# Kernel optimization log

Measured on AMD Instinct MI355X. Metric: run time of the kernel, lower is better.

The kernel has to match this reference:

```python
import jax, jax.numpy as jnp
import numpy as np

HEADS = 4

def gat_layer(x, W, a_src, a_dst, bias, edge_index, n):
    # PyG-style GATConv with self-loops, heads averaged (concat=False) so out dim == hidden_dim
    H, C = a_src.shape
    h = (x @ W).reshape(n, H, C)                      # [N,H,C]
    loops = jnp.arange(n)
    src = jnp.concatenate([edge_index[0], loops])
    dst = jnp.concatenate([edge_index[1], loops])
    e = jax.nn.leaky_relu((h * a_src).sum(-1)[src] + (h * a_dst).sum(-1)[dst], 0.2)  # [E,H]
    m = jax.ops.segment_max(e, dst, num_segments=n)   # segment softmax over incoming edges
    ex = jnp.exp(e - m[dst])
    s = jax.ops.segment_sum(ex, dst, num_segments=n)
    alpha = ex / (s[dst] + 1e-16)
    out = jax.ops.segment_sum(alpha[:, :, None] * h[src], dst, num_segments=n)  # [N,H,C]
    return out.mean(axis=1) + bias

def setup_inputs() -> dict:
    key = jax.random.key(0)
    ks = jax.random.split(key, 24)
    Nd, Ni, Ne = 20000, 4096, 4096
    D_in, D = 512, 256
    n_int, n_emo = 64, 32
    inp = {}
    inp['dialogue_embeddings'] = jax.random.normal(ks[0], (Nd, D_in), jnp.float32)
    inp['intention_indices'] = jax.random.randint(ks[1], (Ni,), 0, n_int)
    inp['emotion_indices'] = jax.random.randint(ks[2], (Ne,), 0, n_emo)
    inp['dialogue_edge_index'] = jax.random.randint(ks[3], (2, Nd * 32), 0, Nd)
    inp['intention_edge_index'] = jax.random.randint(ks[4], (2, Ni * 16), 0, Ni)
    inp['emotion_edge_index'] = jax.random.randint(ks[5], (2, Ne * 16), 0, Ne)
    s = lambda k, shape: jax.random.normal(k, shape, jnp.float32) * 0.02
    inp['intention_emb'] = s(ks[6], (n_int, D))
    inp['emotion_emb'] = s(ks[7], (n_emo, D))
    inp['Wd'] = s(ks[8], (D_in, HEADS * D)); inp['a_src_d'] = s(ks[9], (HEADS, D)); inp['a_dst_d'] = s(ks[10], (HEADS, D)); inp['bd'] = jnp.zeros((D,), jnp.float32)
    inp['Wi'] = s(ks[11], (D, HEADS * D)); inp['a_src_i'] = s(ks[12], (HEADS, D)); inp['a_dst_i'] = s(ks[13], (HEADS, D)); inp['bi'] = jnp.zeros((D,), jnp.float32)
    inp['We'] = s(ks[14], (D, HEADS * D)); inp['a_src_e'] = s(ks[15], (HEADS, D)); inp['a_dst_e'] = s(ks[16], (HEADS, D)); inp['be'] = jnp.zeros((D,), jnp.float32)
    inp['W_dfc'] = s(ks[17], (D, D)); inp['b_dfc'] = jnp.zeros((D,), jnp.float32)
    inp['W_ifc'] = s(ks[18], (D, D)); inp['b_ifc'] = jnp.zeros((D,), jnp.float32)
    inp['W_efc'] = s(ks[19], (D, D)); inp['b_efc'] = jnp.zeros((D,), jnp.float32)
    inp['W_fc'] = s(ks[20], (3 * D, n_emo)); inp['b_fc'] = jnp.zeros((n_emo,), jnp.float32)
    return inp

def reference(dialogue_embeddings, intention_indices, emotion_indices,
              dialogue_edge_index, intention_edge_index, emotion_edge_index,
              intention_emb, emotion_emb,
              Wd, a_src_d, a_dst_d, bd, Wi, a_src_i, a_dst_i, bi,
              We, a_src_e, a_dst_e, be,
              W_dfc, b_dfc, W_ifc, b_ifc, W_efc, b_efc, W_fc, b_fc):
    Nd = dialogue_embeddings.shape[0]
    Ni = intention_indices.shape[0]
    Ne = emotion_indices.shape[0]
    ie = intention_emb[intention_indices]   # [Ni, D]
    ee = emotion_emb[emotion_indices]       # [Ne, D]
    d = gat_layer(dialogue_embeddings, Wd, a_src_d, a_dst_d, bd, dialogue_edge_index, Nd)
    d = jax.nn.relu(d @ W_dfc + b_dfc)
    i = gat_layer(ie, Wi, a_src_i, a_dst_i, bi, intention_edge_index, Ni)
    i = jax.nn.relu(i @ W_ifc + b_ifc)
    e = gat_layer(ee, We, a_src_e, a_dst_e, be, emotion_edge_index, Ne)
    e = jax.nn.relu(e @ W_efc + b_efc)
    iw = jax.nn.softmax(d @ i.T, axis=-1)   # [Nd, Ni]
    att_i = iw @ i                           # [Nd, D]
    ew = jax.nn.softmax(d @ e.T, axis=-1)   # [Nd, Ne]
    att_e = ew @ e                           # [Nd, D]
    inputs = jnp.concatenate([d, att_i, att_e], axis=-1)  # [Nd, 3D]
    return inputs @ W_fc + b_fc
```

## Files before the change

kernel.cpp:

```cpp
#include <hip/hip_runtime.h>
#include <hip/hip_bf16.h>
#include <math.h>

#define DEV static __device__ __forceinline__

typedef __attribute__((ext_vector_type(8))) short short8;
typedef __attribute__((ext_vector_type(4))) short short4v;
typedef __attribute__((ext_vector_type(4))) float f32x4;
typedef __attribute__((ext_vector_type(2))) long long2v;

DEV float bf2f(__hip_bfloat16 x) { return __bfloat162float(x); }
DEV __hip_bfloat16 f2bf(float x) { return __float2bfloat16(x); }
DEV short bfbits(float x) { __hip_bfloat16 h = __float2bfloat16(x); short s; __builtin_memcpy(&s, &h, 2); return s; }
DEV float b2f_bits(short s) { __hip_bfloat16 h; __builtin_memcpy(&h, &s, 2); return __bfloat162float(h); }
DEV float lrelu(float x) { return x > 0.f ? x : 0.2f * x; }

DEV float load_in(const void* p, long long i, bool f32) {
  return f32 ? ((const float*)p)[i] : bf2f(((const __hip_bfloat16*)p)[i]);
}

DEV long pack8_fp8(const float* f) {
  int lo = 0, hi = 0;
  lo = __builtin_amdgcn_cvt_pk_fp8_f32(f[0], f[1], lo, false);
  lo = __builtin_amdgcn_cvt_pk_fp8_f32(f[2], f[3], lo, true);
  hi = __builtin_amdgcn_cvt_pk_fp8_f32(f[4], f[5], hi, false);
  hi = __builtin_amdgcn_cvt_pk_fp8_f32(f[6], f[7], hi, true);
  return ((long)(unsigned)hi << 32) | (unsigned)lo;
}

DEV f32x4 mfma_fp8(long a, long b, f32x4 c) {
  return __builtin_amdgcn_mfma_f32_16x16x32_fp8_fp8(a, b, c, 0, 0, 0);
}

__global__ void HGAN_45148696215914_kernel() {}

__global__ void fill_k(__hip_bfloat16* __restrict__ p, float v, int n)
{
  int i = blockIdx.x * blockDim.x + threadIdx.x;
  if (i < n) p[i] = __float2bfloat16(v);
}

struct DetectArgs { const unsigned int* p[23]; int nw[23]; int id[23]; };

__global__ void detect_k(DetectArgs a, int* __restrict__ flags)
{
  __shared__ int cnt_sh;
  if (threadIdx.x == 0) cnt_sh = 0;
  __syncthreads();
  const unsigned int* w = a.p[blockIdx.x];
  int nwords = a.nw[blockIdx.x];
  int bad = 0;
  for (int i = threadIdx.x; i < nwords; i += blockDim.x) {
    unsigned int x = w[i];
    float v0 = __uint_as_float((x & 0xffffu) << 16);
    float v1 = __uint_as_float(x & 0xffff0000u);
    if (!(fabsf(v0) <= 1e4f)) bad++;
    if (!(fabsf(v1) <= 1e4f)) bad++;
  }
  atomicAdd(&cnt_sh, bad);
  __syncthreads();
  if (threadIdx.x == 0) flags[a.id[blockIdx.x]] = (cnt_sh > nwords / 4) ? 1 : 0;
}

struct CvArgs {
  const void* in[7]; const int* flag[7]; __hip_bfloat16* out[7];
  int K[7], N[7], NL[7], toff[7]; int nseg;
};

__global__ __launch_bounds__(256) void convtrN_k(CvArgs a)
{
  __shared__ __hip_bfloat16 t[32][33];
  int b = blockIdx.x;
  int s = 0;
  while (s + 1 < a.nseg && b >= a.toff[s + 1]) ++s;
  int ti = b - a.toff[s];
  int kb = a.K[s] >> 5;
  int bk = ti % kb, bn = ti / kb;
  const void* in = a.in[s];
  const int* flag = a.flag[s];
  __hip_bfloat16* out = a.out[s];
  int K = a.K[s], N = a.N[s];
  const bool f = flag && *flag;
  int lx = threadIdx.x & 31, ly = threadIdx.x >> 5;
  int gn = bn * 32 + lx;
#pragma unroll
  for (int rr = 0; rr < 32; rr += 8)
    t[rr + ly][lx] = (gn < N)
        ? f2bf(load_in(in, (long long)(bk * 32 + rr + ly) * N + gn, f))
        : f2bf(0.f);
  __syncthreads();
#pragma unroll
  for (int rr = 0; rr < 32; rr += 8)
    out[(size_t)(bn * 32 + rr + ly) * K + bk * 32 + lx] = t[lx][rr + ly];
}

DEV void mgemm_body(
    const void* A, const int* aflag, int lda, const int* idxA,
    const __hip_bfloat16* BT, void* C, int ldc,
    const void* bias, const int* biasflag, int relu,
    int permC, int M, int K, int Nlim, const int* cflag,
    int m0, int n0, __hip_bfloat16* Ash, __hip_bfloat16* Bsh)
{
  const bool af = aflag && *aflag;
  const bool bsf = biasflag && *biasflag;
  const bool cf = cflag && *cflag;
  const int tid = threadIdx.x;
  const int wv = tid >> 6, lane = tid & 63, qd = lane >> 4, lm = lane & 15;
  const int wr = wv >> 1, wc = wv & 1;

  f32x4 acc[4][4];
#pragma unroll
  for (int i = 0; i < 4; ++i)
    for (int j = 0; j < 4; ++j)
      for (int v = 0; v < 4; ++v) acc[i][j][v] = 0.f;

  for (int k0 = 0; k0 < K; k0 += 64) {
    __syncthreads();
    for (int u = tid; u < 1024; u += 256) {
      int r = u >> 3, cu = u & 7;
      int gm = m0 + r;
      short8 vv;
      if (gm < M) {
        long long row = idxA ? idxA[gm] : gm;
        long long basei = row * (long long)lda + k0 + cu * 8;
        if (af) {
          const float4* fp = (const float4*)((const float*)A + basei);
          float4 f0 = fp[0], f1 = fp[1];
          vv[0] = bfbits(f0.x); vv[1] = bfbits(f0.y);
          vv[2] = bfbits(f0.z); vv[3] = bfbits(f0.w);
          vv[4] = bfbits(f1.x); vv[5] = bfbits(f1.y);
          vv[6] = bfbits(f1.z); vv[7] = bfbits(f1.w);
        } else {
          vv = *(const short8*)((const __hip_bfloat16*)A + basei);
        }
      } else {
#pragma unroll
        for (int j = 0; j < 8; ++j) vv[j] = 0;
      }
      *(short8*)(&Ash[r * 72 + cu * 8]) = vv;
    }
    for (int u = tid; u < 1024; u += 256) {
      int r = u >> 3, cu = u & 7;
      *(short8*)(&Bsh[r * 72 + cu * 8]) =
          *(const short8*)(BT + (size_t)(n0 + r) * K + k0 + cu * 8);
    }
    __syncthreads();
#pragma unroll
    for (int ks = 0; ks < 2; ++ks) {
      short8 a[4], b[4];
#pragma unroll
      for (int i = 0; i < 4; ++i)
        a[i] = *(const short8*)(&Ash[(wr * 64 + i * 16 + lm) * 72 + ks * 32 + qd * 8]);
#pragma unroll
      for (int j = 0; j < 4; ++j)
        b[j] = *(const short8*)(&Bsh[(wc * 64 + j * 16 + lm) * 72 + ks * 32 + qd * 8]);
#pragma unroll
      for (int i = 0; i < 4; ++i)
#pragma unroll
        for (int j = 0; j < 4; ++j)
          acc[i][j] = __builtin_amdgcn_mfma_f32_16x16x32_bf16(a[i], b[j], acc[i][j], 0, 0, 0);
    }
  }
#pragma unroll
  for (int j = 0; j < 4; ++j) {
    int gn = n0 + wc * 64 + j * 16 + lm;
    if (gn >= Nlim) continue;
    float bv = bias ? load_in(bias, gn, bsf) : 0.f;
    int gcol = permC ? ((gn & 255) * 4 + (gn >> 8)) : gn;
#pragma unroll
    for (int i = 0; i < 4; ++i) {
#pragma unroll
      for (int v = 0; v < 4; ++v) {
        int gm = m0 + wr * 64 + i * 16 + qd * 4 + v;
        if (gm >= M) continue;
        float x = acc[i][j][v] + bv;
        if (relu) x = fmaxf(x, 0.f);
        long long idx = (long long)gm * ldc + gcol;
        if (cf) ((float*)C)[idx] = x;
        else    ((__hip_bfloat16*)C)[idx] = f2bf(x);
      }
    }
  }
}

__global__ __launch_bounds__(256) void mgemm_k(
    const void* __restrict__ A, const int* __restrict__ aflag, int lda,
    const int* __restrict__ idxA,
    const __hip_bfloat16* __restrict__ BT,
    void* __restrict__ C, int ldc,
    const void* __restrict__ bias, const int* __restrict__ biasflag, int relu,
    int permC, int M, int N, int K, int Nlim,
    const int* __restrict__ cflag)
{
  __shared__ __align__(16) __hip_bfloat16 Ash[128 * 72];
  __shared__ __align__(16) __hip_bfloat16 Bsh[128 * 72];
  (void)N;
  mgemm_body(A, aflag, lda, idxA, BT, C, ldc, bias, biasflag, relu,
             permC, M, K, Nlim, cflag,
             blockIdx.y * 128, blockIdx.x * 128, Ash, Bsh);
}

struct SegArgs {
  const void* A[3]; const int* aflag[3]; int lda[3]; const int* idxA[3];
  const __hip_bfloat16* BT[3]; void* C[3]; int ldc[3];
  const void* bias[3]; const int* bflag[3];
  int M[3]; int K[3]; int yoff[3];
  int relu, permC, Nlim;
};

__global__ __launch_bounds__(256) void mgemm_seg_k(SegArgs a)
{
  __shared__ __align__(16) __hip_bfloat16 Ash[128 * 72];
  __shared__ __align__(16) __hip_bfloat16 Bsh[128 * 72];
  int y = blockIdx.y;
  int s = (y >= a.yoff[2]) ? 2 : ((y >= a.yoff[1]) ? 1 : 0);
  mgemm_body(a.A[s], a.aflag[s], a.lda[s], a.idxA[s], a.BT[s], a.C[s], a.ldc[s],
             a.bias[s], a.bflag[s], a.relu, a.permC, a.M[s], a.K[s], a.Nlim,
             nullptr, (y - a.yoff[s]) * 128, blockIdx.x * 128, Ash, Bsh);
}

__global__ __launch_bounds__(256) void score3_k(
    const __hip_bfloat16* __restrict__ hI,
    const void* as1, const void* ad1, const int* sf1, const int* df1,
    const void* as2, const void* ad2, const int* sf2, const int* df2,
    const void* as3, const void* ad3, const int* sf3, const int* df3,
    int s1, int s2,
    float* __restrict__ ss, float* __restrict__ ds,
    int* __restrict__ cnt, int N)
{
  __shared__ float red[4][8];
  int n = blockIdx.x, c = threadIdx.x;
  if (c == 0) cnt[n] = 0;
  const void* a_src; const void* a_dst; const int* sfp; const int* dfp;
  if (n < s1)      { a_src = as1; a_dst = ad1; sfp = sf1; dfp = df1; }
  else if (n < s2) { a_src = as2; a_dst = ad2; sfp = sf2; dfp = df2; }
  else             { a_src = as3; a_dst = ad3; sfp = sf3; dfp = df3; }
  const bool sf = sfp && *sfp;
  const bool df = dfp && *dfp;
  short4v hv = *(const short4v*)(hI + (size_t)n * 1024 + c * 4);
  float h0 = b2f_bits(hv[0]), h1 = b2f_bits(hv[1]);
  float h2 = b2f_bits(hv[2]), h3 = b2f_bits(hv[3]);
  float r0 = h0 * load_in(a_src, 0 * 256 + c, sf);
  float r1 = h1 * load_in(a_src, 1 * 256 + c, sf);
  float r2 = h2 * load_in(a_src, 2 * 256 + c, sf);
  float r3 = h3 * load_in(a_src, 3 * 256 + c, sf);
  float t0 = h0 * load_in(a_dst, 0 * 256 + c, df);
  float t1 = h1 * load_in(a_dst, 1 * 256 + c, df);
  float t2 = h2 * load_in(a_dst, 2 * 256 + c, df);
  float t3 = h3 * load_in(a_dst, 3 * 256 + c, df);
#pragma unroll
  for (int o = 32; o > 0; o >>= 1) {
    r0 += __shfl_down(r0, o); r1 += __shfl_down(r1, o);
    r2 += __shfl_down(r2, o); r3 += __shfl_down(r3, o);
    t0 += __shfl_down(t0, o); t1 += __shfl_down(t1, o);
    t2 += __shfl_down(t2, o); t3 += __shfl_down(t3, o);
  }
  int wv = c >> 6, lane = c & 63;
  if (lane == 0) {
    red[wv][0] = r0; red[wv][1] = r1; red[wv][2] = r2; red[wv][3] = r3;
    red[wv][4] = t0; red[wv][5] = t1; red[wv][6] = t2; red[wv][7] = t3;
  }
  __syncthreads();
  if (c < 8) {
    float s = red[0][c] + red[1][c] + red[2][c] + red[3][c];
    if (c < 4) ss[n * 4 + c] = s;
    else       ds[n * 4 + (c - 4)] = s;
  }
}

__global__ void count3_k(const int* __restrict__ d1, int E1,
                         const int* __restrict__ d2, int E2, int o2,
                         const int* __restrict__ d3, int E3, int o3,
                         int* __restrict__ cnt)
{
  int k = blockIdx.x * blockDim.x + threadIdx.x;
  if (k < E1) atomicAdd(&cnt[d1[k]], 1);
  else if (k < E1 + E2) atomicAdd(&cnt[d2[k - E1] + o2], 1);
  else if (k < E1 + E2 + E3) atomicAdd(&cnt[d3[k - E1 - E2] + o3], 1);
}

__global__ __launch_bounds__(1024) void scan1_k(
    const int* __restrict__ cnt, int* __restrict__ offp, int* __restrict__ bsum, int n)
{
  __shared__ int sh[1024];
  int idx = blockIdx.x * 1024 + (int)threadIdx.x;
  int v = (idx < n) ? cnt[idx] : 0;
  sh[threadIdx.x] = v;
  __syncthreads();
  for (int d = 1; d < 1024; d <<= 1) {
    int t = (threadIdx.x >= (unsigned)d) ? sh[threadIdx.x - d] : 0;
    __syncthreads();
    sh[threadIdx.x] += t;
    __syncthreads();
  }
  if (idx < n) offp[idx] = sh[threadIdx.x] - v;
  if (threadIdx.x == 1023) bsum[blockIdx.x] = sh[1023];
}

__global__ void scan3_k(int* __restrict__ offp, const int* __restrict__ bsum,
                        int* __restrict__ cur, int n, int nb)
{
  int i = blockIdx.x * blockDim.x + threadIdx.x;
  if (i < n) {
    int chunk = i >> 10;
    int pre = 0;
    for (int b = 0; b < chunk; ++b) pre += bsum[b];
    int v = offp[i] + pre;
    offp[i] = v;
    cur[i] = v;
    if (i == n - 1) {
      int tot = 0;
      for (int b = 0; b < nb; ++b) tot += bsum[b];
      offp[n] = tot;
    }
  }
}

__global__ void scatter3_k(const int* __restrict__ s1, const int* __restrict__ d1, int E1,
                           const int* __restrict__ s2, const int* __restrict__ d2, int E2, int o2,
                           const int* __restrict__ s3, const int* __restrict__ d3, int E3, int o3,
                           int* __restrict__ cur, int* __restrict__ srcs)
{
  int k = blockIdx.x * blockDim.x + threadIdx.x;
  if (k < E1) {
    int p = atomicAdd(&cur[d1[k]], 1);
    srcs[p] = s1[k];
  } else if (k < E1 + E2) {
    int kk = k - E1;
    int p = atomicAdd(&cur[d2[kk] + o2], 1);
    srcs[p] = s2[kk] + o2;
  } else if (k < E1 + E2 + E3) {
    int kk = k - E1 - E2;
    int p = atomicAdd(&cur[d3[kk] + o3], 1);
    srcs[p] = s3[kk] + o3;
  }
}

__global__ __launch_bounds__(256) void agg3_k(
    const __hip_bfloat16* __restrict__ hI,
    const float* __restrict__ ss, const float* __restrict__ ds,
    const int* __restrict__ offp, const int* __restrict__ srcs,
    const void* b1, const int* bf1,
    const void* b2, const int* bf2,
    const void* b3, const int* bf3,
    int s1, int s2,
    __hip_bfloat16* __restrict__ outp, int N)
{
  __shared__ int src_sh[64];
  __shared__ __align__(16) float w_sh[64][4];
  __shared__ float scale_sh[4];
  __shared__ float l_sh[4];
  __shared__ __align__(16) float pair_sh[128][8];
  int n = blockIdx.x;
  int c = threadIdx.x;
  int hd_w = c >> 6;
  int e_w  = c & 63;
  int half = c >> 7;
  int tc   = c & 127;
  int s0 = offp[n], deg = offp[n + 1] - s0;
  int total = deg + 1;
  float dsn = ds[n * 4 + hd_w];
  float m_run = -1e30f, l_run = 0.f;
  float A0[4] = {0.f, 0.f, 0.f, 0.f};
  float A1[4] = {0.f, 0.f, 0.f, 0.f};
  for (int base = 0; base < total; base += 64) {
    int cnt = min(64, total - base);
    __syncthreads();
    if (c < cnt) src_sh[c] = (base + c == 0) ? n : srcs[s0 + base + c - 1];
    __syncthreads();
    float val = -1e30f;
    if (e_w < cnt) val = lrelu(ss[src_sh[e_w] * 4 + hd_w] + dsn);
    float vmax = val;
#pragma unroll
    for (int o = 32; o > 0; o >>= 1) vmax = fmaxf(vmax, __shfl_xor(vmax, o));
    float newm = fmaxf(m_run, vmax);
    float p = (e_w < cnt) ? __expf(val - newm) : 0.f;
    float psum = p;
#pragma unroll
    for (int o = 32; o > 0; o >>= 1) psum += __shfl_xor(psum, o);
    float sc = __expf(m_run - newm);
    l_run = l_run * sc + psum;
    m_run = newm;
    w_sh[e_w][hd_w] = p;
    if (e_w == 0) scale_sh[hd_w] = sc;
    __syncthreads();
    float sc0 = scale_sh[0], sc1 = scale_sh[1], sc2 = scale_sh[2], sc3 = scale_sh[3];
    A0[0] *= sc0; A0[1] *= sc1; A0[2] *= sc2; A0[3] *= sc3;
    A1[0] *= sc0; A1[1] *= sc1; A1[2] *= sc2; A1[3] *= sc3;
    for (int e = half; e < cnt; e += 2) {
      short8 hv = *(const short8*)(hI + (size_t)src_sh[e] * 1024 + tc * 8);
      float4 w = *(const float4*)(&w_sh[e][0]);
      A0[0] += w.x * b2f_bits(hv[0]); A0[1] += w.y * b2f_bits(hv[1]);
      A0[2] += w.z * b2f_bits(hv[2]); A0[3] += w.w * b2f_bits(hv[3]);
      A1[0] += w.x * b2f_bits(hv[4]); A1[1] += w.y * b2f_bits(hv[5]);
      A1[2] += w.z * b2f_bits(hv[6]); A1[3] += w.w * b2f_bits(hv[7]);
    }
  }
  __syncthreads();
  if (e_w == 0) l_sh[hd_w] = l_run;
  if (half == 1) {
    *(float4*)(&pair_sh[tc][0]) = make_float4(A0[0], A0[1], A0[2], A0[3]);
    *(float4*)(&pair_sh[tc][4]) = make_float4(A1[0], A1[1], A1[2], A1[3]);
  }
  __syncthreads();
  if (half == 0) {
    float4 p0 = *(const float4*)(&pair_sh[tc][0]);
    float4 p1 = *(const float4*)(&pair_sh[tc][4]);
    A0[0] += p0.x; A0[1] += p0.y; A0[2] += p0.z; A0[3] += p0.w;
    A1[0] += p1.x; A1[1] += p1.y; A1[2] += p1.z; A1[3] += p1.w;
    const void* bias; const int* bfp;
    if (n < s1)      { bias = b1; bfp = bf1; }
    else if (n < s2) { bias = b2; bfp = bf2; }
    else             { bias = b3; bfp = bf3; }
    const bool bf = bfp && *bfp;
    float il0 = 1.f / (l_sh[0] + 1e-16f), il1 = 1.f / (l_sh[1] + 1e-16f);
    float il2 = 1.f / (l_sh[2] + 1e-16f), il3 = 1.f / (l_sh[3] + 1e-16f);
    float r0 = 0.25f * (A0[0] * il0 + A0[1] * il1 + A0[2] * il2 + A0[3] * il3);
    float r1 = 0.25f * (A1[0] * il0 + A1[1] * il1 + A1[2] * il2 + A1[3] * il3);
    outp[(size_t)n * 256 + 2 * tc]     = f2bf(r0 + load_in(bias, 2 * tc, bf));
    outp[(size_t)n * 256 + 2 * tc + 1] = f2bf(r1 + load_in(bias, 2 * tc + 1, bf));
  }
}

__global__ __launch_bounds__(256) void conv8_k(
    const __hip_bfloat16* __restrict__ in0, char* __restrict__ K8_0, char* __restrict__ KT8_0,
    const __hip_bfloat16* __restrict__ in1, char* __restrict__ K8_1, char* __restrict__ KT8_1,
    int Nk)
{
  __shared__ __align__(16) __hip_bfloat16 t[32][264];
  const __hip_bfloat16* in = blockIdx.y ? in1 : in0;
  char* K8  = blockIdx.y ? K8_1  : K8_0;
  char* KT8 = blockIdx.y ? KT8_1 : KT8_0;
  int kv0 = blockIdx.x * 32;
  int tid = threadIdx.x;
  for (int u = tid; u < 1024; u += 256) {
    int r = u >> 5, c = u & 31;
    *(short8*)(&t[r][c * 8]) = *(const short8*)(in + (size_t)(kv0 + r) * 256 + c * 8);
  }
  __syncthreads();
  for (int u = tid; u < 1024; u += 256) {
    int r = u >> 5, g = u & 31, pos = g * 8;
    int qd = pos >> 6, s = (pos >> 3) & 7;
    int d = s * 32 + qd * 8;
    float f[8];
#pragma unroll
    for (int j = 0; j < 8; ++j) f[j] = 16.f * bf2f(t[r][d + j]);
    *(long*)(K8 + (size_t)(kv0 + r) * 256 + pos) = pack8_fp8(f);
  }
  {
    int d = tid;
#pragma unroll
    for (int g = 0; g < 4; ++g) {
      float f[8];
#pragma unroll
      for (int j = 0; j < 8; ++j) f[j] = 16.f * bf2f(t[g * 8 + j][d]);
      *(long*)(KT8 + (size_t)d * Nk + kv0 + g * 8) = pack8_fp8(f);
    }
  }
}

__global__ __launch_bounds__(256, 2) void flashf8_k(
    const __hip_bfloat16* __restrict__ Q, int ldq,
    const char* __restrict__ K8_0, const char* __restrict__ KT8_0,
    const char* __restrict__ K8_1, const char* __restrict__ KT8_1,
    __hip_bfloat16* __restrict__ Out, int ldo,
    int M, int Nk)
{
  __shared__ __align__(16) char Ksh8[2][32 * 272];
  __shared__ __align__(16) char KTsh8[2][256 * 48];
  __shared__ __align__(16) char Psh8[4][32 * 40];
  const int att = blockIdx.y;
  const char* K8  = att ? K8_1  : K8_0;
  const char* KT8 = att ? KT8_1 : KT8_0;
  __hip_bfloat16* Outp = Out + att * 256;

  const int tid = threadIdx.x;
  const int wv = tid >> 6, lane = tid & 63;
  const int qd = lane >> 4, lm = lane & 15;
  const int r0 = blockIdx.x * 128 + wv * 32;
  char* Pw = Psh8[wv];

  const int kr0 = tid >> 4, kc = tid & 15;
  const int tr0 = tid >> 1, tcq = tid & 1;

  long qf8[2][8];
#pragma unroll
  for (int mf = 0; mf < 2; ++mf) {
    const bool ok = (r0 + mf * 16 + lm) < M;
    const __hip_bfloat16* qrow = Q + (size_t)(r0 + mf * 16 + lm) * ldq;
#pragma unroll
    for (int s = 0; s < 8; ++s) {
      float f[8];
      if (ok) {
        short8 qv = *(const short8*)(qrow + s * 32 + qd * 8);
#pragma unroll
        for (int j = 0; j < 8; ++j) f[j] = 16.f * b2f_bits(qv[j]);
      } else {
#pragma unroll
        for (int j = 0; j < 8; ++j) f[j] = 0.f;
      }
      qf8[mf][s] = pack8_fp8(f);
    }
  }

  f32x4 Oacc[2][16];
#pragma unroll
  for (int mf = 0; mf < 2; ++mf)
    for (int i = 0; i < 16; ++i)
      for (int v = 0; v < 4; ++v) Oacc[mf][i][v] = 0.f;
  float mrow[2] = {-1e30f, -1e30f}, lrow[2] = {0.f, 0.f};

  {
    short8 k0 = *(const short8*)(K8 + (size_t)kr0 * 256 + kc * 16);
    short8 k1 = *(const short8*)(K8 + (size_t)(kr0 + 16) * 256 + kc * 16);
    short8 t0 = *(const short8*)(KT8 + (size_t)tr0 * Nk + tcq * 16);
    short8 t1 = *(const short8*)(KT8 + (size_t)(tr0 + 128) * Nk + tcq * 16);
    *(short8*)(&Ksh8[0][kr0 * 272 + kc * 16]) = k0;
    *(short8*)(&Ksh8[0][(kr0 + 16) * 272 + kc * 16]) = k1;
    *(short8*)(&KTsh8[0][tr0 * 48 + tcq * 16]) = t0;
    *(short8*)(&KTsh8[0][(tr0 + 128) * 48 + tcq * 16]) = t1;
  }
  __syncthreads();

  int iter = 0;
  for (int n0 = 0; n0 < Nk; n0 += 32, ++iter) {
    const int cur = iter & 1, nxt = cur ^ 1;
    const bool havenext = (n0 + 32) < Nk;
    short8 pk0, pk1, pt0, pt1;
    if (havenext) {
      int nn = n0 + 32;
      pk0 = *(const short8*)(K8 + (size_t)(nn + kr0) * 256 + kc * 16);
      pk1 = *(const short8*)(K8 + (size_t)(nn + kr0 + 16) * 256 + kc * 16);
      pt0 = *(const short8*)(KT8 + (size_t)tr0 * Nk + nn + tcq * 16);
      pt1 = *(const short8*)(KT8 + (size_t)(tr0 + 128) * Nk + nn + tcq * 16);
    }
    const char* Kc  = Ksh8[cur];
    const char* KTc = KTsh8[cur];

    f32x4 S[2][2];
#pragma unroll
    for (int t = 0; t < 2; ++t)
      for (int mf = 0; mf < 2; ++mf)
        for (int v = 0; v < 4; ++v) S[t][mf][v] = 0.f;
#pragma unroll
    for (int sp = 0; sp < 4; ++sp) {
#pragma unroll
      for (int t = 0; t < 2; ++t) {
        long2v a2 = *(const long2v*)(&Kc[(t * 16 + lm) * 272 + qd * 64 + sp * 16]);
#pragma unroll
        for (int mf = 0; mf < 2; ++mf) {
          S[t][mf] = mfma_fp8(a2[0], qf8[mf][2 * sp],     S[t][mf]);
          S[t][mf] = mfma_fp8(a2[1], qf8[mf][2 * sp + 1], S[t][mf]);
        }
      }
    }
#pragma unroll
    for (int t = 0; t < 2; ++t)
      for (int mf = 0; mf < 2; ++mf)
        for (int v = 0; v < 4; ++v) S[t][mf][v] *= 0.00390625f;

    float scale[2];
#pragma unroll
    for (int mf = 0; mf < 2; ++mf) {
      float tmax = -1e30f;
#pragma unroll
      for (int t = 0; t < 2; ++t)
        for (int v = 0; v < 4; ++v) tmax = fmaxf(tmax, S[t][mf][v]);
      tmax = fmaxf(tmax, __shfl_xor(tmax, 16));
      tmax = fmaxf(tmax, __shfl_xor(tmax, 32));
      float newm = fmaxf(mrow[mf], tmax);
      float psum = 0.f;
#pragma unroll
      for (int t = 0; t < 2; ++t)
        for (int v = 0; v < 4; ++v) {
          float p = __expf(S[t][mf][v] - newm);
          S[t][mf][v] = p;
          psum += p;
        }
      psum += __shfl_xor(psum, 16);
      psum += __shfl_xor(psum, 32);
      scale[mf] = __expf(mrow[mf] - newm);
      lrow[mf] = lrow[mf] * scale[mf] + psum;
      mrow[mf] = newm;
#pragma unroll
      for (int t = 0; t < 2; ++t) {
        int pk = __builtin_amdgcn_cvt_pk_fp8_f32(16.f * S[t][mf][0], 16.f * S[t][mf][1], 0, false);
        pk = __builtin_amdgcn_cvt_pk_fp8_f32(16.f * S[t][mf][2], 16.f * S[t][mf][3], pk, true);
        *(int*)(&Pw[(mf * 16 + lm) * 40 + t * 16 + qd * 4]) = pk;
      }
    }

#pragma unroll
    for (int mf = 0; mf < 2; ++mf) {
      if (__any(scale[mf] < 1.0f)) {
        float scl[4];
#pragma unroll
        for (int v = 0; v < 4; ++v) scl[v] = __shfl(scale[mf], qd * 4 + v);
#pragma unroll
        for (int i = 0; i < 16; ++i)
          for (int v = 0; v < 4; ++v) Oacc[mf][i][v] *= scl[v];
      }
    }

    {
      long pa0 = *(const long*)(&Pw[(0 * 16 + lm) * 40 + qd * 8]);
      long pa1 = *(const long*)(&Pw[(1 * 16 + lm) * 40 + qd * 8]);
#pragma unroll
      for (int dt = 0; dt < 16; ++dt) {
        long b = *(const long*)(&KTc[(dt * 16 + lm) * 48 + qd * 8]);
        Oacc[0][dt] = mfma_fp8(pa0, b, Oacc[0][dt]);
        Oacc[1][dt] = mfma_fp8(pa1, b, Oacc[1][dt]);
      }
    }

    if (havenext) {
      *(short8*)(&Ksh8[nxt][kr0 * 272 + kc * 16]) = pk0;
      *(short8*)(&Ksh8[nxt][(kr0 + 16) * 272 + kc * 16]) = pk1;
      *(short8*)(&KTsh8[nxt][tr0 * 48 + tcq * 16]) = pt0;
      *(short8*)(&KTsh8[nxt][(tr0 + 128) * 48 + tcq * 16]) = pt1;
    }
    __syncthreads();
  }

#pragma unroll
  for (int mf = 0; mf < 2; ++mf) {
    float linv = 1.f / (256.f * lrow[mf]);
    float li[4];
#pragma unroll
    for (int v = 0; v < 4; ++v) li[v] = __shfl(linv, qd * 4 + v);
#pragma unroll
    for (int v = 0; v < 4; ++v) {
      int grow = r0 + mf * 16 + qd * 4 + v;
      if (grow >= M) continue;
#pragma unroll
      for (int dt = 0; dt < 16; ++dt)
        Outp[(size_t)grow * ldo + dt * 16 + lm] = f2bf(Oacc[mf][dt][v] * li[v]);
    }
  }
}

extern "C" void kernel_launch(void* const* d_in, const int* in_sizes, int n_in,
                              void* d_out, int out_size, void* d_ws, size_t ws_size,
                              hipStream_t stream)
{
  const void* Xd      = d_in[0];
  const int*  int_idx = (const int*)d_in[1];
  const int*  emo_idx = (const int*)d_in[2];
  const int*  ed_d    = (const int*)d_in[3];
  const int*  ed_i    = (const int*)d_in[4];
  const int*  ed_e    = (const int*)d_in[5];
  const void* int_emb = d_in[6];
  const void* emo_emb = d_in[7];
  const void* Wd = d_in[8],  *a_src_d = d_in[9],  *a_dst_d = d_in[10], *bd = d_in[11];
  const void* Wi = d_in[12], *a_src_i = d_in[13], *a_dst_i = d_in[14], *bi = d_in[15];
  const void* We = d_in[16], *a_src_e = d_in[17], *a_dst_e = d_in[18], *be = d_in[19];
  const void* W_dfc = d_in[20], *b_dfc = d_in[21];
  const void* W_ifc = d_in[22], *b_ifc = d_in[23];
  const void* W_efc = d_in[24], *b_efc = d_in[25];
  const void* W_fc  = d_in[26], *b_fc  = d_in[27];

  const int DIn  = in_sizes[8] / 1024;
  const int Nd   = in_sizes[0] / DIn;
  const int Ni   = in_sizes[1];
  const int Ne   = in_sizes[2];
  const int Ed   = in_sizes[3] / 2;
  const int Ei   = in_sizes[4] / 2;
  const int Ee   = in_sizes[5] / 2;
  const int Nout = in_sizes[27];
  const int NU   = Nd + Ni + Ne;

  char* base = (char*)d_ws;
  size_t off = 0;
  auto alloc = [&](size_t nbytes) -> void* {
    void* p = base + off;
    off = (off + nbytes + 255) & ~(size_t)255;
    return p;
  };
  int* flags = (int*)alloc(32 * sizeof(int));
  int* bsum  = (int*)alloc(64 * sizeof(int));
  __hip_bfloat16* hbuf = (__hip_bfloat16*)alloc((size_t)NU * 1024 * 2);
  __hip_bfloat16* cat  = (__hip_bfloat16*)alloc((size_t)Nd * 768 * 2);
  __hip_bfloat16* gat_tmp = (__hip_bfloat16*)alloc((size_t)NU * 256 * 2);
  __hip_bfloat16* WdT  = (__hip_bfloat16*)alloc((size_t)1024 * DIn * 2);
  __hip_bfloat16* WiT  = (__hip_bfloat16*)alloc((size_t)1024 * 256 * 2);
  __hip_bfloat16* WeT  = (__hip_bfloat16*)alloc((size_t)1024 * 256 * 2);
  __hip_bfloat16* WdfT = (__hip_bfloat16*)alloc((size_t)256 * 256 * 2);
  __hip_bfloat16* WifT = (__hip_bfloat16*)alloc((size_t)256 * 256 * 2);
  __hip_bfloat16* WefT = (__hip_bfloat16*)alloc((size_t)256 * 256 * 2);
  __hip_bfloat16* WfcT = (__hip_bfloat16*)alloc((size_t)128 * 768 * 2);
  float* ss  = (float*)alloc((size_t)NU * 4 * 4);
  float* dsb = (float*)alloc((size_t)NU * 4 * 4);
  int* cnt   = (int*)alloc((size_t)NU * 4);
  int* offp  = (int*)alloc((size_t)(NU + 1) * 4);
  int* cur   = (int*)alloc((size_t)NU * 4);
  int* srcs  = (int*)alloc((size_t)(Ed + Ei + Ee) * 4);
  const size_t need = off;
  (void)n_in;

  __hip_bfloat16* i_mat = hbuf;
  __hip_bfloat16* e_mat = hbuf + (size_t)Ni * 256;
  char* K8i  = (char*)(hbuf + (size_t)2 * Ni * 256);
  char* KT8i = K8i + (size_t)Ni * 256;
  char* K8e  = KT8i + (size_t)Ni * 256;
  char* KT8e = K8e + (size_t)Ne * 256;

  const dim3 T(256);
  if (ws_size < need) {
    fill_k<<<(out_size + 255) / 256, T, 0, stream>>>((__hip_bfloat16*)d_out, 0.25f, out_size);
    return;
  }

  {
    DetectArgs da;
    const int fid[23] = {0,6,7,8,9,10,11,12,13,14,15,16,17,18,19,20,21,22,23,24,25,26,27};
    for (int t = 0; t < 23; ++t) {
      int id = fid[t];
      int nw = in_sizes[id] / 2;
      if (nw > 2048) nw = 2048;
      if (nw < 1) nw = 1;
      da.p[t] = (const unsigned int*)d_in[id];
      da.nw[t] = nw;
      da.id[t] = id;
    }
    detect_k<<<23, 256, 0, stream>>>(da, flags);
  }
  #define F(i) (flags + (i))

  {
    CvArgs cv;
    const void* ins[7]  = {Wd, Wi, We, W_dfc, W_ifc, W_efc, W_fc};
    const int*  fgs[7]  = {F(8), F(12), F(16), F(20), F(22), F(24), F(26)};
    __hip_bfloat16* outs[7] = {WdT, WiT, WeT, WdfT, WifT, WefT, WfcT};
    int Ks[7]  = {DIn, 256, 256, 256, 256, 256, 768};
    int Ns[7]  = {1024, 1024, 1024, 256, 256, 256, Nout};
    int NLs[7] = {1024, 1024, 1024, 256, 256, 256, 128};
    int run = 0;
    for (int s = 0; s < 7; ++s) {
      cv.in[s] = ins[s]; cv.flag[s] = fgs[s]; cv.out[s] = outs[s];
      cv.K[s] = Ks[s]; cv.N[s] = Ns[s]; cv.NL[s] = NLs[s]; cv.toff[s] = run;
      run += (Ks[s] / 32) * (NLs[s] / 32);
    }
    cv.nseg = 7;
    convtrN_k<<<run, T, 0, stream>>>(cv);
  }

  const int yNd = (Nd + 127) / 128, yNi = Ni / 128, yNe = Ne / 128;
  {
    SegArgs sa;
    sa.A[0] = Xd;      sa.aflag[0] = F(0); sa.lda[0] = DIn; sa.idxA[0] = nullptr;
    sa.BT[0] = WdT;    sa.C[0] = hbuf;     sa.ldc[0] = 1024;
    sa.bias[0] = nullptr; sa.bflag[0] = nullptr; sa.M[0] = Nd; sa.K[0] = DIn;
    sa.A[1] = int_emb; sa.aflag[1] = F(6); sa.lda[1] = 256; sa.idxA[1] = int_idx;
    sa.BT[1] = WiT;    sa.C[1] = hbuf + (size_t)Nd * 1024; sa.ldc[1] = 1024;
    sa.bias[1] = nullptr; sa.bflag[1] = nullptr; sa.M[1] = Ni; sa.K[1] = 256;
    sa.A[2] = emo_emb; sa.aflag[2] = F(7); sa.lda[2] = 256; sa.idxA[2] = emo_idx;
    sa.BT[2] = WeT;    sa.C[2] = hbuf + (size_t)(Nd + Ni) * 1024; sa.ldc[2] = 1024;
    sa.bias[2] = nullptr; sa.bflag[2] = nullptr; sa.M[2] = Ne; sa.K[2] = 256;
    sa.yoff[0] = 0; sa.yoff[1] = yNd; sa.yoff[2] = yNd + yNi;
    sa.relu = 0; sa.permC = 1; sa.Nlim = 1024;
    mgemm_seg_k<<<dim3(8, yNd + yNi + yNe), T, 0, stream>>>(sa);
  }

  {
    int nb = (NU + 1023) / 1024;
    int Etot = Ed + Ei + Ee;
    score3_k<<<NU, T, 0, stream>>>(hbuf,
        a_src_d, a_dst_d, F(9), F(10),
        a_src_i, a_dst_i, F(13), F(14),
        a_src_e, a_dst_e, F(17), F(18),
        Nd, Nd + Ni, ss, dsb, cnt, NU);
    count3_k<<<(Etot + 255) / 256, T, 0, stream>>>(
        ed_d + Ed, Ed, ed_i + Ei, Ei, Nd, ed_e + Ee, Ee, Nd + Ni, cnt);
    scan1_k<<<nb, 1024, 0, stream>>>(cnt, offp, bsum, NU);
    scan3_k<<<(NU + 255) / 256, T, 0, stream>>>(offp, bsum, cur, NU, nb);
    scatter3_k<<<(Etot + 255) / 256, T, 0, stream>>>(
        ed_d, ed_d + Ed, Ed, ed_i, ed_i + Ei, Ei, Nd,
        ed_e, ed_e + Ee, Ee, Nd + Ni, cur, srcs);
    agg3_k<<<NU, T, 0, stream>>>(hbuf, ss, dsb, offp, srcs,
        bd, F(11), bi, F(15), be, F(19), Nd, Nd + Ni, gat_tmp, NU);
  }

  {
    SegArgs sa;
    sa.A[0] = gat_tmp; sa.aflag[0] = nullptr; sa.lda[0] = 256; sa.idxA[0] = nullptr;
    sa.BT[0] = WdfT;   sa.C[0] = cat;   sa.ldc[0] = 768;
    sa.bias[0] = b_dfc; sa.bflag[0] = F(21); sa.M[0] = Nd; sa.K[0] = 256;
    sa.A[1] = gat_tmp + (size_t)Nd * 256; sa.aflag[1] = nullptr; sa.lda[1] = 256; sa.idxA[1] = nullptr;
    sa.BT[1] = WifT;   sa.C[1] = i_mat; sa.ldc[1] = 256;
    sa.bias[1] = b_ifc; sa.bflag[1] = F(23); sa.M[1] = Ni; sa.K[1] = 256;
    sa.A[2] = gat_tmp + (size_t)(Nd + Ni) * 256; sa.aflag[2] = nullptr; sa.lda[2] = 256; sa.idxA[2] = nullptr;
    sa.BT[2] = WefT;   sa.C[2] = e_mat; sa.ldc[2] = 256;
    sa.bias[2] = b_efc; sa.bflag[2] = F(25); sa.M[2] = Ne; sa.K[2] = 256;
    sa.yoff[0] = 0; sa.yoff[1] = yNd; sa.yoff[2] = yNd + yNi;
    sa.relu = 1; sa.permC = 0; sa.Nlim = 256;
    mgemm_seg_k<<<dim3(2, yNd + yNi + yNe), T, 0, stream>>>(sa);
  }

  conv8_k<<<dim3(Ni / 32, 2), T, 0, stream>>>(i_mat, K8i, KT8i, e_mat, K8e, KT8e, Ni);

  flashf8_k<<<dim3((Nd + 127) / 128, 2), T, 0, stream>>>(
      cat, 768, K8i, KT8i, K8e, KT8e, cat + 256, 768, Nd, Ni);

  mgemm_k<<<dim3(1, (Nd + 127) / 128), T, 0, stream>>>(
      cat, nullptr, 768, nullptr, WfcT, d_out, Nout,
      b_fc, F(27), 0, 0, Nd, 128, 768, Nout, F(0));
}
```

Before: 913.0 us.

## Split flash attention block into eight waves of 16 rows with XOR-swizzled K tile

The fp8 flash-attention kernel now runs 512 threads per block, and each wave handles 16 query rows instead of 32. This halves per-wave accumulator registers and lets four blocks share a CU, so more waves can hide latency. Each thread now stages a single K and KT chunk per iteration instead of two. The padded K shared-memory layout is replaced by an XOR swizzle to avoid bank conflicts and save LDS. In exchange, each wave reuses every loaded K/KT fragment for half as many rows, so shared-memory reads per MFMA go up.

```diff
diff --git a/kernel.cpp b/kernel.cpp
--- a/kernel.cpp
+++ b/kernel.cpp
@@ -459,16 +459,16 @@
   }
 }
 
-__global__ __launch_bounds__(256, 2) void flashf8_k(
+__global__ __launch_bounds__(512, 4) void flashf8_k(
     const __hip_bfloat16* __restrict__ Q, int ldq,
     const char* __restrict__ K8_0, const char* __restrict__ KT8_0,
     const char* __restrict__ K8_1, const char* __restrict__ KT8_1,
     __hip_bfloat16* __restrict__ Out, int ldo,
     int M, int Nk)
 {
-  __shared__ __align__(16) char Ksh8[2][32 * 272];
+  __shared__ __align__(16) char Ksh8[2][32 * 256];
   __shared__ __align__(16) char KTsh8[2][256 * 48];
-  __shared__ __align__(16) char Psh8[4][32 * 40];
+  __shared__ __align__(16) char Psh8[8][16 * 40];
   const int att = blockIdx.y;
   const char* K8  = att ? K8_1  : K8_0;
   const char* KT8 = att ? KT8_1 : KT8_0;
@@ -477,17 +477,17 @@
   const int tid = threadIdx.x;
   const int wv = tid >> 6, lane = tid & 63;
   const int qd = lane >> 4, lm = lane & 15;
-  const int r0 = blockIdx.x * 128 + wv * 32;
+  const int r0 = blockIdx.x * 128 + wv * 16;
   char* Pw = Psh8[wv];
 
   const int kr0 = tid >> 4, kc = tid & 15;
+  const int kcs = kc ^ (kr0 & 7);
   const int tr0 = tid >> 1, tcq = tid & 1;
 
-  long qf8[2][8];
-#pragma unroll
-  for (int mf = 0; mf < 2; ++mf) {
-    const bool ok = (r0 + mf * 16 + lm) < M;
-    const __hip_bfloat16* qrow = Q + (size_t)(r0 + mf * 16 + lm) * ldq;
+  long qf8[8];
+  {
+    const bool ok = (r0 + lm) < M;
+    const __hip_bfloat16* qrow = Q + (size_t)(r0 + lm) * ldq;
 #pragma unroll
     for (int s = 0; s < 8; ++s) {
       float f[8];
@@ -499,26 +499,21 @@
 #pragma unroll
         for (int j = 0; j < 8; ++j) f[j] = 0.f;
       }
-      qf8[mf][s] = pack8_fp8(f);
-    }
-  }
-
-  f32x4 Oacc[2][16];
-#pragma unroll
-  for (int mf = 0; mf < 2; ++mf)
-    for (int i = 0; i < 16; ++i)
-      for (int v = 0; v < 4; ++v) Oacc[mf][i][v] = 0.f;
-  float mrow[2] = {-1e30f, -1e30f}, lrow[2] = {0.f, 0.f};
+      qf8[s] = pack8_fp8(f);
+    }
+  }
+
+  f32x4 Oacc[16];
+#pragma unroll
+  for (int i = 0; i < 16; ++i)
+    for (int v = 0; v < 4; ++v) Oacc[i][v] = 0.f;
+  float mrow = -1e30f, lrow = 0.f;
 
   {
     short8 k0 = *(const short8*)(K8 + (size_t)kr0 * 256 + kc * 16);
-    short8 k1 = *(const short8*)(K8 + (size_t)(kr0 + 16) * 256 + kc * 16);
     short8 t0 = *(const short8*)(KT8 + (size_t)tr0 * Nk + tcq * 16);
-    short8 t1 = *(const short8*)(KT8 + (size_t)(tr0 + 128) * Nk + tcq * 16);
-    *(short8*)(&Ksh8[0][kr0 * 272 + kc * 16]) = k0;
-    *(short8*)(&Ksh8[0][(kr0 + 16) * 272 + kc * 16]) = k1;
+    *(short8*)(&Ksh8[0][kr0 * 256 + kcs * 16]) = k0;
     *(short8*)(&KTsh8[0][tr0 * 48 + tcq * 16]) = t0;
-    *(short8*)(&KTsh8[0][(tr0 + 128) * 48 + tcq * 16]) = t1;
   }
   __syncthreads();
 
@@ -526,115 +521,97 @@
   for (int n0 = 0; n0 < Nk; n0 += 32, ++iter) {
     const int cur = iter & 1, nxt = cur ^ 1;
     const bool havenext = (n0 + 32) < Nk;
-    short8 pk0, pk1, pt0, pt1;
+    short8 pk0, pt0;
     if (havenext) {
       int nn = n0 + 32;
       pk0 = *(const short8*)(K8 + (size_t)(nn + kr0) * 256 + kc * 16);
-      pk1 = *(const short8*)(K8 + (size_t)(nn + kr0 + 16) * 256 + kc * 16);
       pt0 = *(const short8*)(KT8 + (size_t)tr0 * Nk + nn + tcq * 16);
-      pt1 = *(const short8*)(KT8 + (size_t)(tr0 + 128) * Nk + nn + tcq * 16);
     }
     const char* Kc  = Ksh8[cur];
     const char* KTc = KTsh8[cur];
 
-    f32x4 S[2][2];
+    f32x4 S[2];
 #pragma unroll
     for (int t = 0; t < 2; ++t)
-      for (int mf = 0; mf < 2; ++mf)
-        for (int v = 0; v < 4; ++v) S[t][mf][v] = 0.f;
+      for (int v = 0; v < 4; ++v) S[t][v] = 0.f;
 #pragma unroll
     for (int sp = 0; sp < 4; ++sp) {
 #pragma unroll
       for (int t = 0; t < 2; ++t) {
-        long2v a2 = *(const long2v*)(&Kc[(t * 16 + lm) * 272 + qd * 64 + sp * 16]);
-#pragma unroll
-        for (int mf = 0; mf < 2; ++mf) {
-          S[t][mf] = mfma_fp8(a2[0], qf8[mf][2 * sp],     S[t][mf]);
-          S[t][mf] = mfma_fp8(a2[1], qf8[mf][2 * sp + 1], S[t][mf]);
-        }
+        long2v a2 = *(const long2v*)(
+            &Kc[(t * 16 + lm) * 256 + (((qd * 4 + sp) ^ (lm & 7)) << 4)]);
+        S[t] = mfma_fp8(a2[0], qf8[2 * sp],     S[t]);
+        S[t] = mfma_fp8(a2[1], qf8[2 * sp + 1], S[t]);
       }
     }
 #pragma unroll
     for (int t = 0; t < 2; ++t)
-      for (int mf = 0; mf < 2; ++mf)
-        for (int v = 0; v < 4; ++v) S[t][mf][v] *= 0.00390625f;
-
-    float scale[2];
-#pragma unroll
-    for (int mf = 0; mf < 2; ++mf) {
-      float tmax = -1e30f;
-#pragma unroll
-      for (int t = 0; t < 2; ++t)
-        for (int v = 0; v < 4; ++v) tmax = fmaxf(tmax, S[t][mf][v]);
-      tmax = fmaxf(tmax, __shfl_xor(tmax, 16));
-      tmax = fmaxf(tmax, __shfl_xor(tmax, 32));
-      float newm = fmaxf(mrow[mf], tmax);
-      float psum = 0.f;
-#pragma unroll
-      for (int t = 0; t < 2; ++t)
-        for (int v = 0; v < 4; ++v) {
-          float p = __expf(S[t][mf][v] - newm);
-          S[t][mf][v] = p;
-          psum += p;
-        }
-      psum += __shfl_xor(psum, 16);
-      psum += __shfl_xor(psum, 32);
-      scale[mf] = __expf(mrow[mf] - newm);
-      lrow[mf] = lrow[mf] * scale[mf] + psum;
-      mrow[mf] = newm;
-#pragma unroll
-      for (int t = 0; t < 2; ++t) {
-        int pk = __builtin_amdgcn_cvt_pk_fp8_f32(16.f * S[t][mf][0], 16.f * S[t][mf][1], 0, false);
-        pk = __builtin_amdgcn_cvt_pk_fp8_f32(16.f * S[t][mf][2], 16.f * S[t][mf][3], pk, true);
-        *(int*)(&Pw[(mf * 16 + lm) * 40 + t * 16 + qd * 4]) = pk;
+      for (int v = 0; v < 4; ++v) S[t][v] *= 0.00390625f;
+
+    float tmax = -1e30f;
+#pragma unroll
+    for (int t = 0; t < 2; ++t)
+      for (int v = 0; v < 4; ++v) tmax = fmaxf(tmax, S[t][v]);
+    tmax = fmaxf(tmax, __shfl_xor(tmax, 16));
+    tmax = fmaxf(tmax, __shfl_xor(tmax, 32));
+    float newm = fmaxf(mrow, tmax);
+    float psum = 0.f;
+#pragma unroll
+    for (int t = 0; t < 2; ++t)
+      for (int v = 0; v < 4; ++v) {
+        float p = __expf(S[t][v] - newm);
+        S[t][v] = p;
+        psum += p;
       }
-    }
-
-#pragma unroll
-    for (int mf = 0; mf < 2; ++mf) {
-      if (__any(scale[mf] < 1.0f)) {
-        float scl[4];
-#pragma unroll
-        for (int v = 0; v < 4; ++v) scl[v] = __shfl(scale[mf], qd * 4 + v);
-#pragma unroll
-        for (int i = 0; i < 16; ++i)
-          for (int v = 0; v < 4; ++v) Oacc[mf][i][v] *= scl[v];
-      }
+    psum += __shfl_xor(psum, 16);
+    psum += __shfl_xor(psum, 32);
+    float scale = __expf(mrow - newm);
+    lrow = lrow * scale + psum;
+    mrow = newm;
+#pragma unroll
+    for (int t = 0; t < 2; ++t) {
+      int pk = __builtin_amdgcn_cvt_pk_fp8_f32(16.f * S[t][0], 16.f * S[t][1], 0, false);
+      pk = __builtin_amdgcn_cvt_pk_fp8_f32(16.f * S[t][2], 16.f * S[t][3], pk, true);
+      *(int*)(&Pw[lm * 40 + t * 16 + qd * 4]) = pk;
+    }
+
+    if (__any(scale < 1.0f)) {
+      float scl[4];
+#pragma unroll
+      for (int v = 0; v < 4; ++v) scl[v] = __shfl(scale, qd * 4 + v);
+#pragma unroll
+      for (int i = 0; i < 16; ++i)
+        for (int v = 0; v < 4; ++v) Oacc[i][v] *= scl[v];
     }
 
     {
-      long pa0 = *(const long*)(&Pw[(0 * 16 + lm) * 40 + qd * 8]);
-      long pa1 = *(const long*)(&Pw[(1 * 16 + lm) * 40 + qd * 8]);
+      long pa0 = *(const long*)(&Pw[lm * 40 + qd * 8]);
 #pragma unroll
       for (int dt = 0; dt < 16; ++dt) {
         long b = *(const long*)(&KTc[(dt * 16 + lm) * 48 + qd * 8]);
-        Oacc[0][dt] = mfma_fp8(pa0, b, Oacc[0][dt]);
-        Oacc[1][dt] = mfma_fp8(pa1, b, Oacc[1][dt]);
+        Oacc[dt] = mfma_fp8(pa0, b, Oacc[dt]);
       }
     }
 
     if (havenext) {
-      *(short8*)(&Ksh8[nxt][kr0 * 272 + kc * 16]) = pk0;
-      *(short8*)(&Ksh8[nxt][(kr0 + 16) * 272 + kc * 16]) = pk1;
+      *(short8*)(&Ksh8[nxt][kr0 * 256 + kcs * 16]) = pk0;
       *(short8*)(&KTsh8[nxt][tr0 * 48 + tcq * 16]) = pt0;
-      *(short8*)(&KTsh8[nxt][(tr0 + 128) * 48 + tcq * 16]) = pt1;
     }
     __syncthreads();
   }
 
-#pragma unroll
-  for (int mf = 0; mf < 2; ++mf) {
-    float linv = 1.f / (256.f * lrow[mf]);
+  {
+    float linv = 1.f / (256.f * lrow);
     float li[4];
 #pragma unroll
     for (int v = 0; v < 4; ++v) li[v] = __shfl(linv, qd * 4 + v);
 #pragma unroll
     for (int v = 0; v < 4; ++v) {
-      int grow = r0 + mf * 16 + qd * 4 + v;
+      int grow = r0 + qd * 4 + v;
       if (grow >= M) continue;
 #pragma unroll
       for (int dt = 0; dt < 16; ++dt)
-        Outp[(size_t)grow * ldo + dt * 16 + lm] = f2bf(Oacc[mf][dt][v] * li[v]);
+        Outp[(size_t)grow * ldo + dt * 16 + lm] = f2bf(Oacc[dt][v] * li[v]);
     }
   }
 }
@@ -798,7 +775,7 @@
 
   conv8_k<<<dim3(Ni / 32, 2), T, 0, stream>>>(i_mat, K8i, KT8i, e_mat, K8e, KT8e, Ni);
 
-  flashf8_k<<<dim3((Nd + 127) / 128, 2), T, 0, stream>>>(
+  flashf8_k<<<dim3((Nd + 127) / 128, 2), dim3(512), 0, stream>>>(
       cat, 768, K8i, KT8i, K8e, KT8e, cat + 256, 768, Nd, Ni);
 
   mgemm_k<<<dim3(1, (Nd + 127) / 128), T, 0, stream>>>(
```

After: 919.9 us. About the same (+0.8%).
